# Performance work log

Measured on AMD Instinct MI355X. Metric: run time of the kernel, lower is better.

Reference implementation:

```python
import jax, jax.numpy as jnp
import numpy as np

N_NODES = 50000
N_EDGES = 800000
D = 96        # node feature dim (init arg D)
C = 16        # number of classes
BN_EPS = 1e-5


def _mlp_layer(x, w, b, g, beta):
    # Linear -> ReLU -> BatchNorm1d (training-mode batch stats, biased var)
    h = jax.nn.relu(x @ w + b)
    mu = h.mean(axis=0)
    var = h.var(axis=0)
    return g * (h - mu) * jax.lax.rsqrt(var + BN_EPS) + beta


def _gine_conv(x, e, src, dst, w, b, g, beta):
    # PyG GINEConv (eps=0): nn((1+eps)*x + sum_j ReLU(x_j + e_ij))
    msg = jax.nn.relu(x[src] + e)                      # [E, D] gather + edge add
    agg = jax.ops.segment_sum(msg, dst, num_segments=N_NODES)  # scatter-add
    return _mlp_layer(x + agg, w, b, g, beta)


def setup_inputs() -> dict:
    ks = jax.random.split(jax.random.key(0), 16)

    def p(k, shape, fan_in):
        return jax.random.normal(k, shape, jnp.float32) * (1.0 / np.sqrt(fan_in))

    inp = {
        "x": jax.random.normal(ks[0], (N_NODES, D), jnp.float32),
        "edge_attr": jax.random.normal(ks[1], (N_EDGES, 1), jnp.float32),
        "edge_index": jax.random.randint(ks[2], (2, N_EDGES), 0, N_NODES, jnp.int32),
        # fresh Linear(1, D) applied to edge_attr in forward
        "lin_w": p(ks[3], (1, D), 1), "lin_b": jnp.zeros((D,), jnp.float32),
        # conv1: GINEConv(MLP([D, D]))
        "conv1_w": p(ks[4], (D, D), D), "conv1_b": jnp.zeros((D,), jnp.float32),
        "conv1_g": jnp.ones((D,), jnp.float32), "conv1_beta": jnp.zeros((D,), jnp.float32),
        # conv2: GINEConv(MLP([D, 64]))
        "conv2_w": p(ks[5], (D, 64), D), "conv2_b": jnp.zeros((64,), jnp.float32),
        "conv2_g": jnp.ones((64,), jnp.float32), "conv2_beta": jnp.zeros((64,), jnp.float32),
        # lin1: MLP([D+64, 96])
        "lin1_w": p(ks[6], (D + 64, 96), D + 64), "lin1_b": jnp.zeros((96,), jnp.float32),
        "lin1_g": jnp.ones((96,), jnp.float32), "lin1_beta": jnp.zeros((96,), jnp.float32),
        # mlp1: MLP([96, 96, C]) -> two Linear+ReLU+BN layers
        "mlp1a_w": p(ks[7], (96, 96), 96), "mlp1a_b": jnp.zeros((96,), jnp.float32),
        "mlp1a_g": jnp.ones((96,), jnp.float32), "mlp1a_beta": jnp.zeros((96,), jnp.float32),
        "mlp1b_w": p(ks[8], (96, C), 96), "mlp1b_b": jnp.zeros((C,), jnp.float32),
        "mlp1b_g": jnp.ones((C,), jnp.float32), "mlp1b_beta": jnp.zeros((C,), jnp.float32),
    }
    return inp


def reference(x, edge_attr, edge_index,
              lin_w, lin_b,
              conv1_w, conv1_b, conv1_g, conv1_beta,
              conv2_w, conv2_b, conv2_g, conv2_beta,
              lin1_w, lin1_b, lin1_g, lin1_beta,
              mlp1a_w, mlp1a_b, mlp1a_g, mlp1a_beta,
              mlp1b_w, mlp1b_b, mlp1b_g, mlp1b_beta):
    src, dst = edge_index[0], edge_index[1]
    # D_n(=96) > D_e(=1): edge_attr lifted to [E, D] by Linear(1, D)
    e = edge_attr @ lin_w + lin_b                      # [E, D]
    x1 = _gine_conv(x, e, src, dst, conv1_w, conv1_b, conv1_g, conv1_beta)   # [N, D]
    x2 = _gine_conv(x1, e, src, dst, conv2_w, conv2_b, conv2_g, conv2_beta)  # [N, 64]
    h = _mlp_layer(jnp.concatenate([x1, x2], axis=1), lin1_w, lin1_b, lin1_g, lin1_beta)  # [N, 96]
    # task='node', G=0 -> no pooling, no global features
    h = _mlp_layer(h, mlp1a_w, mlp1a_b, mlp1a_g, mlp1a_beta)
    out = _mlp_layer(h, mlp1b_w, mlp1b_b, mlp1b_g, mlp1b_beta)               # [N, C]
    return out
```

## Files before the change

### kernel.cpp

```cpp
#include <hip/hip_runtime.h>

#define NN 50000
#define NE 800000
#define DD 96
#define BN_EPS 1e-5
#define NB 196

typedef __attribute__((ext_vector_type(8))) short short8v;
typedef __attribute__((ext_vector_type(4))) float float4v;

__device__ inline float bf2f(unsigned u) { return __uint_as_float(u << 16); }
__device__ inline unsigned short f2bf(float f) {
  unsigned u = __float_as_uint(f);
  return (unsigned short)((u + 0x7FFF + ((u >> 16) & 1)) >> 16);
}
__device__ inline void unpack8(uint4 v, float* f) {
  f[0] = bf2f(v.x & 0xffff); f[1] = bf2f(v.x >> 16);
  f[2] = bf2f(v.y & 0xffff); f[3] = bf2f(v.y >> 16);
  f[4] = bf2f(v.z & 0xffff); f[5] = bf2f(v.z >> 16);
  f[6] = bf2f(v.w & 0xffff); f[7] = bf2f(v.w >> 16);
}
__device__ inline uint4 pack8(const float* f) {
  uint4 v;
  v.x = (unsigned)f2bf(f[0]) | ((unsigned)f2bf(f[1]) << 16);
  v.y = (unsigned)f2bf(f[2]) | ((unsigned)f2bf(f[3]) << 16);
  v.z = (unsigned)f2bf(f[4]) | ((unsigned)f2bf(f[5]) << 16);
  v.w = (unsigned)f2bf(f[6]) | ((unsigned)f2bf(f[7]) << 16);
  return v;
}

__global__ __launch_bounds__(256) void f2bf_k(const float* __restrict__ in,
                                              unsigned short* __restrict__ out,
                                              int n8) {
  int t = blockIdx.x * 256 + threadIdx.x;
  if (t >= n8) return;
  const float4* p = (const float4*)in + 2 * t;
  float4 a = p[0], b = p[1];
  float f[8] = {a.x, a.y, a.z, a.w, b.x, b.y, b.z, b.w};
  ((uint4*)out)[t] = pack8(f);
}

__global__ __launch_bounds__(256) void hist_rank(const int* __restrict__ dst,
                                                 int* __restrict__ counts,
                                                 int* __restrict__ rank) {
  int e = blockIdx.x * 256 + threadIdx.x;
  if (e < NE) rank[e] = atomicAdd(&counts[dst[e]], 1);
}

__global__ __launch_bounds__(256) void scan_part(const int* __restrict__ counts,
                                                 int* __restrict__ bsum) {
  __shared__ int s[256];
  int tid = threadIdx.x;
  int i = blockIdx.x * 256 + tid;
  s[tid] = (i < NN) ? counts[i] : 0;
  __syncthreads();
  for (int st = 128; st > 0; st >>= 1) {
    if (tid < st) s[tid] += s[tid + st];
    __syncthreads();
  }
  if (tid == 0) bsum[blockIdx.x] = s[0];
}

__global__ __launch_bounds__(256) void scan_top(const int* __restrict__ bsum,
                                                int* __restrict__ boff) {
  __shared__ int s[256];
  int tid = threadIdx.x;
  int v = (tid < NB) ? bsum[tid] : 0;
  s[tid] = v;
  __syncthreads();
  for (int off = 1; off < 256; off <<= 1) {
    int t = (tid >= off) ? s[tid - off] : 0;
    __syncthreads();
    s[tid] += t;
    __syncthreads();
  }
  if (tid < NB) boff[tid] = s[tid] - v;
}

__global__ __launch_bounds__(256) void scan_apply(
    const int* __restrict__ counts, const int* __restrict__ boff,
    int* __restrict__ rowstart) {
  __shared__ int s[256];
  int tid = threadIdx.x;
  int i = blockIdx.x * 256 + tid;
  int v = (i < NN) ? counts[i] : 0;
  s[tid] = v;
  __syncthreads();
  for (int off = 1; off < 256; off <<= 1) {
    int t = (tid >= off) ? s[tid - off] : 0;
    __syncthreads();
    s[tid] += t;
    __syncthreads();
  }
  if (i < NN) rowstart[i] = boff[blockIdx.x] + s[tid] - v;
  if (i == 0) rowstart[NN] = NE;
}

__global__ __launch_bounds__(256) void scatter_k(
    const int* __restrict__ src, const int* __restrict__ dst,
    const float* __restrict__ ea, const int* __restrict__ rowstart,
    const int* __restrict__ rank, unsigned* __restrict__ pack) {
  int e = blockIdx.x * 256 + threadIdx.x;
  if (e >= NE) return;
  int p = rowstart[dst[e]] + rank[e];
  pack[p] = (unsigned)src[e] | ((unsigned)f2bf(ea[e]) << 16);
}

__global__ __launch_bounds__(256) void agg_wave(
    const unsigned short* __restrict__ xin, const float* __restrict__ lw,
    const float* __restrict__ lb, const int* __restrict__ rowstart,
    const unsigned* __restrict__ pack, unsigned short* __restrict__ out) {
  int n = blockIdx.x * 4 + (threadIdx.x >> 6);
  int lane = threadIdx.x & 63;
  int es = lane / 12;
  int c8 = lane - es * 12;
  float lwv[8], lbv[8], acc[8];
#pragma unroll
  for (int i = 0; i < 8; i++) {
    lwv[i] = lw[c8 * 8 + i];
    lbv[i] = lb[c8 * 8 + i];
    acc[i] = 0.f;
  }
  if (es == 0) {
    uint4 xo = *(const uint4*)(xin + (size_t)n * DD + c8 * 8);
    unpack8(xo, acc);
  }
  int beg = rowstart[n], end = rowstart[n + 1];
  if (lane < 60) {
    int i = beg + es;
    for (; i + 5 < end; i += 10) {
      unsigned pk0 = pack[i], pk1 = pack[i + 5];
      float ev0 = bf2f(pk0 >> 16), ev1 = bf2f(pk1 >> 16);
      uint4 xv0 = *(const uint4*)(xin + (size_t)(pk0 & 0xffff) * DD + c8 * 8);
      uint4 xv1 = *(const uint4*)(xin + (size_t)(pk1 & 0xffff) * DD + c8 * 8);
      float xs0[8], xs1[8];
      unpack8(xv0, xs0);
      unpack8(xv1, xs1);
#pragma unroll
      for (int j = 0; j < 8; j++) {
        acc[j] += fmaxf(xs0[j] + fmaf(ev0, lwv[j], lbv[j]), 0.0f);
        acc[j] += fmaxf(xs1[j] + fmaf(ev1, lwv[j], lbv[j]), 0.0f);
      }
    }
    if (i < end) {
      unsigned pk = pack[i];
      float ev = bf2f(pk >> 16);
      uint4 xv = *(const uint4*)(xin + (size_t)(pk & 0xffff) * DD + c8 * 8);
      float xs[8];
      unpack8(xv, xs);
#pragma unroll
      for (int j = 0; j < 8; j++)
        acc[j] += fmaxf(xs[j] + fmaf(ev, lwv[j], lbv[j]), 0.0f);
    }
  }
#pragma unroll
  for (int j = 0; j < 8; j++) {
    float a = acc[j];
    float t1 = __shfl_down(a, 12);
    float t2 = __shfl_down(a, 24);
    float t3 = __shfl_down(a, 36);
    float t4 = __shfl_down(a, 48);
    acc[j] = a + t1 + t2 + t3 + t4;
  }
  if (es == 0)
    *(uint4*)(out + (size_t)n * DD + c8 * 8) = pack8(acc);
}

__global__ __launch_bounds__(256) void agg_wave_norm(
    const unsigned short* __restrict__ h, const double* __restrict__ st,
    const float* __restrict__ g, const float* __restrict__ be,
    const float* __restrict__ lw, const float* __restrict__ lb,
    const int* __restrict__ rowstart, const unsigned* __restrict__ pack,
    unsigned short* __restrict__ out) {
  __shared__ float scs[96], shs[96];
  int tid = threadIdx.x;
  if (tid < 96) {
    double mu = st[tid] / (double)NN;
    double var = st[96 + tid] / (double)NN - mu * mu;
    double inv = 1.0 / sqrt(var + (double)BN_EPS);
    double sc = (double)g[tid] * inv;
    scs[tid] = (float)sc;
    shs[tid] = (float)((double)be[tid] - mu * sc);
  }
  __syncthreads();
  int n = blockIdx.x * 4 + (tid >> 6);
  int lane = tid & 63;
  int es = lane / 12;
  int c8 = lane - es * 12;
  float sc[8], tsh[8], tlb[8], lwv[8], acc[8];
#pragma unroll
  for (int i = 0; i < 8; i++) {
    sc[i] = scs[c8 * 8 + i];
    tsh[i] = shs[c8 * 8 + i];
    tlb[i] = tsh[i] + lb[c8 * 8 + i];
    lwv[i] = lw[c8 * 8 + i];
    acc[i] = 0.f;
  }
  if (es == 0) {
    uint4 xo = *(const uint4*)(h + (size_t)n * DD + c8 * 8);
    float f[8];
    unpack8(xo, f);
#pragma unroll
    for (int i = 0; i < 8; i++) acc[i] = fmaf(sc[i], f[i], tsh[i]);
  }
  int beg = rowstart[n], end = rowstart[n + 1];
  if (lane < 60) {
    int i = beg + es;
    for (; i + 5 < end; i += 10) {
      unsigned pk0 = pack[i], pk1 = pack[i + 5];
      float ev0 = bf2f(pk0 >> 16), ev1 = bf2f(pk1 >> 16);
      uint4 xv0 = *(const uint4*)(h + (size_t)(pk0 & 0xffff) * DD + c8 * 8);
      uint4 xv1 = *(const uint4*)(h + (size_t)(pk1 & 0xffff) * DD + c8 * 8);
      float xs0[8], xs1[8];
      unpack8(xv0, xs0);
      unpack8(xv1, xs1);
#pragma unroll
      for (int j = 0; j < 8; j++) {
        acc[j] += fmaxf(fmaf(sc[j], xs0[j], fmaf(ev0, lwv[j], tlb[j])), 0.0f);
        acc[j] += fmaxf(fmaf(sc[j], xs1[j], fmaf(ev1, lwv[j], tlb[j])), 0.0f);
      }
    }
    if (i < end) {
      unsigned pk = pack[i];
      float ev = bf2f(pk >> 16);
      uint4 xv = *(const uint4*)(h + (size_t)(pk & 0xffff) * DD + c8 * 8);
      float xs[8];
      unpack8(xv, xs);
#pragma unroll
      for (int j = 0; j < 8; j++)
        acc[j] += fmaxf(fmaf(sc[j], xs[j], fmaf(ev, lwv[j], tlb[j])), 0.0f);
    }
  }
#pragma unroll
  for (int j = 0; j < 8; j++) {
    float a = acc[j];
    float t1 = __shfl_down(a, 12);
    float t2 = __shfl_down(a, 24);
    float t3 = __shfl_down(a, 36);
    float t4 = __shfl_down(a, 48);
    acc[j] = a + t1 + t2 + t3 + t4;
  }
  if (es == 0)
    *(uint4*)(out + (size_t)n * DD + c8 * 8) = pack8(acc);
}

template <int K, int M, int KA, int KB>
__global__ __launch_bounds__(256) void wprep(
    const float* __restrict__ W, const float* __restrict__ b,
    const double* __restrict__ stA, const float* __restrict__ gA,
    const float* __restrict__ beA, const double* __restrict__ stB,
    const float* __restrict__ gB, const float* __restrict__ beB,
    unsigned short* __restrict__ Wz, float* __restrict__ bf) {
  constexpr int KT = K / 32, MT = M / 16;
  __shared__ float scA[KA > 0 ? KA : 1], shA[KA > 0 ? KA : 1];
  __shared__ float scB[KB > 0 ? KB : 1], shB[KB > 0 ? KB : 1];
  int tid = threadIdx.x;
  if (KA > 0 && tid < KA) {
    double mu = stA[tid] / (double)NN;
    double var = stA[KA + tid] / (double)NN - mu * mu;
    double inv = 1.0 / sqrt(var + (double)BN_EPS);
    double sc = (double)gA[tid] * inv;
    scA[tid] = (float)sc;
    shA[tid] = (float)((double)beA[tid] - mu * sc);
  }
  if (KB > 0 && tid < KB) {
    double mu = stB[tid] / (double)NN;
    double var = stB[KB + tid] / (double)NN - mu * mu;
    double inv = 1.0 / sqrt(var + (double)BN_EPS);
    double sc = (double)gB[tid] * inv;
    scB[tid] = (float)sc;
    shB[tid] = (float)((double)beB[tid] - mu * sc);
  }
  if (KA > 0 || KB > 0) __syncthreads();

  int t = blockIdx.x * 256 + tid;
  if (t < KT * MT * 64) {
    int lane = t & 63, fr = t >> 6;
    int kt = fr / MT, ct = fr - kt * MT;
    int col = ct * 16 + (lane & 15);
    int k0 = kt * 32 + (lane >> 4) * 8;
    float f[8];
#pragma unroll
    for (int j = 0; j < 8; j++) {
      int k = k0 + j;
      float w = W[k * M + col];
      if (KA > 0 && k < KA) w *= scA[k];
      if (KB > 0 && k >= KA && k < KA + KB) w *= scB[k - KA];
      f[j] = w;
    }
    ((uint4*)Wz)[t] = pack8(f);
  } else if (t < KT * MT * 64 + M) {
    int j = t - KT * MT * 64;
    float acc = b[j];
    if (KA > 0)
      for (int k = 0; k < KA; k++) acc += shA[k] * W[k * M + j];
    if (KB > 0)
      for (int k = 0; k < KB; k++) acc += shB[k] * W[(KA + k) * M + j];
    bf[j] = acc;
  }
}

template <int K1, int K2, int M, bool OUTF32>
__global__ __launch_bounds__(256) void gemm_mfma(
    const unsigned short* __restrict__ A1,
    const unsigned short* __restrict__ A2,
    const unsigned short* __restrict__ Wz, const float* __restrict__ bias,
    void* __restrict__ hOut, double* __restrict__ stats) {
  constexpr int K = K1 + K2;
  constexpr int KT = K / 32;
  constexpr int MT = M / 16;
  constexpr int NT = NN / 16;
  int tid = threadIdx.x;
  int wave = tid >> 6, lane = tid & 63;
  int lr = lane & 15, lk = lane >> 4;

  float bj[MT], s[MT], q[MT];
#pragma unroll
  for (int ct = 0; ct < MT; ct++) {
    bj[ct] = bias[ct * 16 + lr];
    s[ct] = 0.f;
    q[ct] = 0.f;
  }

  for (int tt = blockIdx.x * 4 + wave; tt < NT; tt += gridDim.x * 4) {
    float4v acc[MT];
#pragma unroll
    for (int ct = 0; ct < MT; ct++) acc[ct] = (float4v){0.f, 0.f, 0.f, 0.f};

    const unsigned short* a1 = A1 + (size_t)(tt * 16 + lr) * K1 + lk * 8;
    const unsigned short* a2 =
        (K2 > 0) ? A2 + (size_t)(tt * 16 + lr) * K2 + lk * 8 : a1;
#pragma unroll
    for (int kt = 0; kt < KT; kt++) {
      short8v av;
      if (kt * 32 < K1)
        av = *reinterpret_cast<const short8v*>(a1 + kt * 32);
      else
        av = *reinterpret_cast<const short8v*>(a2 + (kt * 32 - K1));
#pragma unroll
      for (int ct = 0; ct < MT; ct++) {
        short8v bv = *reinterpret_cast<const short8v*>(
            Wz + ((size_t)(kt * MT + ct) * 64 + lane) * 8);
        acc[ct] =
            __builtin_amdgcn_mfma_f32_16x16x32_bf16(av, bv, acc[ct], 0, 0, 0);
      }
    }
#pragma unroll
    for (int ct = 0; ct < MT; ct++) {
#pragma unroll
      for (int i = 0; i < 4; i++) {
        float o = fmaxf(acc[ct][i] + bj[ct], 0.f);
        size_t row = (size_t)tt * 16 + lk * 4 + i;
        if (OUTF32)
          ((float*)hOut)[row * M + ct * 16 + lr] = o;
        else
          ((unsigned short*)hOut)[row * M + ct * 16 + lr] = f2bf(o);
        s[ct] += o;
        q[ct] += o * o;
      }
    }
  }

  __shared__ float sred[4][M], qred[4][M];
#pragma unroll
  for (int ct = 0; ct < MT; ct++) {
    float ss = s[ct], qq = q[ct];
    ss += __shfl_xor(ss, 16);
    ss += __shfl_xor(ss, 32);
    qq += __shfl_xor(qq, 16);
    qq += __shfl_xor(qq, 32);
    if (lk == 0) {
      sred[wave][ct * 16 + lr] = ss;
      qred[wave][ct * 16 + lr] = qq;
    }
  }
  __syncthreads();
  if (tid < M) {
    double ss = (double)sred[0][tid] + sred[1][tid] + sred[2][tid] + sred[3][tid];
    double qq = (double)qred[0][tid] + qred[1][tid] + qred[2][tid] + qred[3][tid];
    atomicAdd(&stats[tid], ss);
    atomicAdd(&stats[M + tid], qq);
  }
}

__global__ __launch_bounds__(256) void bnout(const float4* __restrict__ h,
                                             const double* __restrict__ stats,
                                             const float* __restrict__ g,
                                             const float* __restrict__ beta,
                                             float4* __restrict__ out) {
  __shared__ float sc[16], sh[16];
  int tid = threadIdx.x;
  if (tid < 16) {
    double mu = stats[tid] / (double)NN;
    double var = stats[16 + tid] / (double)NN - mu * mu;
    double inv = 1.0 / sqrt(var + (double)BN_EPS);
    double scale = (double)g[tid] * inv;
    sc[tid] = (float)scale;
    sh[tid] = (float)((double)beta[tid] - mu * scale);
  }
  __syncthreads();
  int t = blockIdx.x * 256 + tid;
  if (t >= NN * 4) return;
  float4 v = h[t];
  int j0 = (4 * t) & 15;
  float4 o;
  o.x = fmaf(v.x, sc[j0 + 0], sh[j0 + 0]);
  o.y = fmaf(v.y, sc[j0 + 1], sh[j0 + 1]);
  o.z = fmaf(v.z, sc[j0 + 2], sh[j0 + 2]);
  o.w = fmaf(v.w, sc[j0 + 3], sh[j0 + 3]);
  out[t] = o;
}

static inline char* alignup(char* p, size_t a) {
  return (char*)(((uintptr_t)p + a - 1) & ~(uintptr_t)(a - 1));
}

extern "C" void kernel_launch(void* const* d_in, const int* in_sizes, int n_in,
                              void* d_out, int out_size, void* d_ws,
                              size_t ws_size, hipStream_t stream) {
  const float* x = (const float*)d_in[0];
  const float* ea = (const float*)d_in[1];
  const int* ei = (const int*)d_in[2];
  const int* src = ei;
  const int* dst = ei + NE;
  const float* lin_w = (const float*)d_in[3];
  const float* lin_b = (const float*)d_in[4];
  const float* c1_w = (const float*)d_in[5];
  const float* c1_b = (const float*)d_in[6];
  const float* c1_g = (const float*)d_in[7];
  const float* c1_be = (const float*)d_in[8];
  const float* c2_w = (const float*)d_in[9];
  const float* c2_b = (const float*)d_in[10];
  const float* c2_g = (const float*)d_in[11];
  const float* c2_be = (const float*)d_in[12];
  const float* l1_w = (const float*)d_in[13];
  const float* l1_b = (const float*)d_in[14];
  const float* l1_g = (const float*)d_in[15];
  const float* l1_be = (const float*)d_in[16];
  const float* ma_w = (const float*)d_in[17];
  const float* ma_b = (const float*)d_in[18];
  const float* ma_g = (const float*)d_in[19];
  const float* ma_be = (const float*)d_in[20];
  const float* mb_w = (const float*)d_in[21];
  const float* mb_b = (const float*)d_in[22];
  const float* mb_g = (const float*)d_in[23];
  const float* mb_be = (const float*)d_in[24];

  typedef unsigned short us;
  char* p = (char*)d_ws;
  us* xb = (us*)p;   p += (size_t)NN * 96 * 2;
  us* Ab = (us*)p;   p += (size_t)NN * 96 * 2;
  us* H1 = (us*)p;   p += (size_t)NN * 96 * 2;
  us* H2 = (us*)p;   p += (size_t)NN * 64 * 2;
  us* H3 = (us*)p;   p += (size_t)NN * 96 * 2;
  us* H4 = (us*)p;   p += (size_t)NN * 96 * 2;
  float* H5 = (float*)p; p += (size_t)NN * 16 * 4;
  p = alignup(p, 256);
  us* Wz1 = (us*)p;  p += 3 * 6 * 64 * 8 * 2;
  us* Wz2 = (us*)p;  p += 3 * 4 * 64 * 8 * 2;
  us* Wz3 = (us*)p;  p += 5 * 6 * 64 * 8 * 2;
  us* Wz4 = (us*)p;  p += 3 * 6 * 64 * 8 * 2;
  us* Wz5 = (us*)p;  p += 3 * 1 * 64 * 8 * 2;
  p = alignup(p, 256);
  float* bf1 = (float*)p; p += 96 * 4;
  float* bf2 = (float*)p; p += 64 * 4;
  float* bf3 = (float*)p; p += 96 * 4;
  float* bf4 = (float*)p; p += 96 * 4;
  float* bf5 = (float*)p; p += 16 * 4;
  p = alignup(p, 256);
  char* zbase = p;
  int* counts = (int*)p;  p += (size_t)NN * 4;
  double* stats = (double*)p; p += (size_t)5 * 192 * 8;
  size_t zbytes = (size_t)(p - zbase);
  int* rowstart = (int*)p; p += (size_t)(NN + 1) * 4;
  int* bsum = (int*)p;    p += 256 * 4;
  int* boff = (int*)p;    p += 256 * 4;
  int* rank = (int*)p;    p += (size_t)NE * 4;
  unsigned* pack = (unsigned*)p; p += (size_t)NE * 4;

  hipMemsetAsync(zbase, 0, zbytes, stream);

  const int eb = (NE + 255) / 256;
  const int n12 = NN * 12;
  const int b12 = (n12 + 255) / 256;
  const int aggG = NN / 4;
  const int GG = 782;

  f2bf_k<<<b12, 256, 0, stream>>>(x, xb, n12);
  hist_rank<<<eb, 256, 0, stream>>>(dst, counts, rank);
  scan_part<<<NB, 256, 0, stream>>>(counts, bsum);
  scan_top<<<1, 256, 0, stream>>>(bsum, boff);
  scan_apply<<<NB, 256, 0, stream>>>(counts, boff, rowstart);
  scatter_k<<<eb, 256, 0, stream>>>(src, dst, ea, rowstart, rank, pack);

  agg_wave<<<aggG, 256, 0, stream>>>(xb, lin_w, lin_b, rowstart, pack, Ab);
  wprep<96, 96, 0, 0><<<5, 256, 0, stream>>>(
      c1_w, c1_b, nullptr, nullptr, nullptr, nullptr, nullptr, nullptr, Wz1,
      bf1);
  gemm_mfma<96, 0, 96, false><<<GG, 256, 0, stream>>>(Ab, nullptr, Wz1, bf1,
                                                      H1, stats);

  agg_wave_norm<<<aggG, 256, 0, stream>>>(H1, stats, c1_g, c1_be, lin_w, lin_b,
                                          rowstart, pack, Ab);
  wprep<96, 64, 0, 0><<<4, 256, 0, stream>>>(
      c2_w, c2_b, nullptr, nullptr, nullptr, nullptr, nullptr, nullptr, Wz2,
      bf2);
  gemm_mfma<96, 0, 64, false><<<GG, 256, 0, stream>>>(Ab, nullptr, Wz2, bf2,
                                                      H2, stats + 192);

  wprep<160, 96, 96, 64><<<8, 256, 0, stream>>>(l1_w, l1_b, stats, c1_g, c1_be,
                                                stats + 192, c2_g, c2_be, Wz3,
                                                bf3);
  gemm_mfma<96, 64, 96, false><<<GG, 256, 0, stream>>>(H1, H2, Wz3, bf3, H3,
                                                       stats + 384);

  wprep<96, 96, 96, 0><<<5, 256, 0, stream>>>(ma_w, ma_b, stats + 384, l1_g,
                                              l1_be, nullptr, nullptr, nullptr,
                                              Wz4, bf4);
  gemm_mfma<96, 0, 96, false><<<GG, 256, 0, stream>>>(H3, nullptr, Wz4, bf4,
                                                      H4, stats + 576);

  wprep<96, 16, 96, 0><<<1, 256, 0, stream>>>(mb_w, mb_b, stats + 576, ma_g,
                                              ma_be, nullptr, nullptr, nullptr,
                                              Wz5, bf5);
  gemm_mfma<96, 0, 16, true><<<GG, 256, 0, stream>>>(H4, nullptr, Wz5, bf5, H5,
                                                     stats + 768);
  bnout<<<(NN * 4 + 255) / 256, 256, 0, stream>>>(
      (const float4*)H5, stats + 768, mb_g, mb_be, (float4*)d_out);
}
```

Baseline: 369.7 us.

## Replace double atomic BN stats with per-block partials and a reduction kernel

```diff
diff --git a/kernel.cpp b/kernel.cpp
--- a/kernel.cpp
+++ b/kernel.cpp
@@ -5,6 +5,7 @@
 #define DD 96
 #define BN_EPS 1e-5
 #define NB 196
+#define GGEMM 782
 
 typedef __attribute__((ext_vector_type(8))) short short8v;
 typedef __attribute__((ext_vector_type(4))) float float4v;
@@ -167,31 +168,19 @@
 }
 
 __global__ __launch_bounds__(256) void agg_wave_norm(
-    const unsigned short* __restrict__ h, const double* __restrict__ st,
-    const float* __restrict__ g, const float* __restrict__ be,
+    const unsigned short* __restrict__ h, const float* __restrict__ coeff,
     const float* __restrict__ lw, const float* __restrict__ lb,
     const int* __restrict__ rowstart, const unsigned* __restrict__ pack,
     unsigned short* __restrict__ out) {
-  __shared__ float scs[96], shs[96];
-  int tid = threadIdx.x;
-  if (tid < 96) {
-    double mu = st[tid] / (double)NN;
-    double var = st[96 + tid] / (double)NN - mu * mu;
-    double inv = 1.0 / sqrt(var + (double)BN_EPS);
-    double sc = (double)g[tid] * inv;
-    scs[tid] = (float)sc;
-    shs[tid] = (float)((double)be[tid] - mu * sc);
-  }
-  __syncthreads();
-  int n = blockIdx.x * 4 + (tid >> 6);
-  int lane = tid & 63;
+  int n = blockIdx.x * 4 + (threadIdx.x >> 6);
+  int lane = threadIdx.x & 63;
   int es = lane / 12;
   int c8 = lane - es * 12;
   float sc[8], tsh[8], tlb[8], lwv[8], acc[8];
 #pragma unroll
   for (int i = 0; i < 8; i++) {
-    sc[i] = scs[c8 * 8 + i];
-    tsh[i] = shs[c8 * 8 + i];
+    sc[i] = coeff[c8 * 8 + i];
+    tsh[i] = coeff[96 + c8 * 8 + i];
     tlb[i] = tsh[i] + lb[c8 * 8 + i];
     lwv[i] = lw[c8 * 8 + i];
     acc[i] = 0.f;
@@ -245,35 +234,14 @@
 }
 
 template <int K, int M, int KA, int KB>
-__global__ __launch_bounds__(256) void wprep(
-    const float* __restrict__ W, const float* __restrict__ b,
-    const double* __restrict__ stA, const float* __restrict__ gA,
-    const float* __restrict__ beA, const double* __restrict__ stB,
-    const float* __restrict__ gB, const float* __restrict__ beB,
-    unsigned short* __restrict__ Wz, float* __restrict__ bf) {
+__global__ __launch_bounds__(256) void wprep(const float* __restrict__ W,
+                                             const float* __restrict__ b,
+                                             const float* __restrict__ cA,
+                                             const float* __restrict__ cB,
+                                             unsigned short* __restrict__ Wz,
+                                             float* __restrict__ bf) {
   constexpr int KT = K / 32, MT = M / 16;
-  __shared__ float scA[KA > 0 ? KA : 1], shA[KA > 0 ? KA : 1];
-  __shared__ float scB[KB > 0 ? KB : 1], shB[KB > 0 ? KB : 1];
-  int tid = threadIdx.x;
-  if (KA > 0 && tid < KA) {
-    double mu = stA[tid] / (double)NN;
-    double var = stA[KA + tid] / (double)NN - mu * mu;
-    double inv = 1.0 / sqrt(var + (double)BN_EPS);
-    double sc = (double)gA[tid] * inv;
-    scA[tid] = (float)sc;
-    shA[tid] = (float)((double)beA[tid] - mu * sc);
-  }
-  if (KB > 0 && tid < KB) {
-    double mu = stB[tid] / (double)NN;
-    double var = stB[KB + tid] / (double)NN - mu * mu;
-    double inv = 1.0 / sqrt(var + (double)BN_EPS);
-    double sc = (double)gB[tid] * inv;
-    scB[tid] = (float)sc;
-    shB[tid] = (float)((double)beB[tid] - mu * sc);
-  }
-  if (KA > 0 || KB > 0) __syncthreads();
-
-  int t = blockIdx.x * 256 + tid;
+  int t = blockIdx.x * 256 + threadIdx.x;
   if (t < KT * MT * 64) {
     int lane = t & 63, fr = t >> 6;
     int kt = fr / MT, ct = fr - kt * MT;
@@ -284,8 +252,8 @@
     for (int j = 0; j < 8; j++) {
       int k = k0 + j;
       float w = W[k * M + col];
-      if (KA > 0 && k < KA) w *= scA[k];
-      if (KB > 0 && k >= KA && k < KA + KB) w *= scB[k - KA];
+      if (KA > 0 && k < KA) w *= cA[k];
+      if (KB > 0 && k >= KA && k < KA + KB) w *= cB[k - KA];
       f[j] = w;
     }
     ((uint4*)Wz)[t] = pack8(f);
@@ -293,9 +261,9 @@
     int j = t - KT * MT * 64;
     float acc = b[j];
     if (KA > 0)
-      for (int k = 0; k < KA; k++) acc += shA[k] * W[k * M + j];
+      for (int k = 0; k < KA; k++) acc += cA[KA + k] * W[k * M + j];
     if (KB > 0)
-      for (int k = 0; k < KB; k++) acc += shB[k] * W[(KA + k) * M + j];
+      for (int k = 0; k < KB; k++) acc += cB[KB + k] * W[(KA + k) * M + j];
     bf[j] = acc;
   }
 }
@@ -305,7 +273,7 @@
     const unsigned short* __restrict__ A1,
     const unsigned short* __restrict__ A2,
     const unsigned short* __restrict__ Wz, const float* __restrict__ bias,
-    void* __restrict__ hOut, double* __restrict__ stats) {
+    void* __restrict__ hOut, float* __restrict__ partial) {
   constexpr int K = K1 + K2;
   constexpr int KT = K / 32;
   constexpr int MT = M / 16;
@@ -376,38 +344,50 @@
   }
   __syncthreads();
   if (tid < M) {
-    double ss = (double)sred[0][tid] + sred[1][tid] + sred[2][tid] + sred[3][tid];
-    double qq = (double)qred[0][tid] + qred[1][tid] + qred[2][tid] + qred[3][tid];
-    atomicAdd(&stats[tid], ss);
-    atomicAdd(&stats[M + tid], qq);
+    partial[(size_t)blockIdx.x * (2 * M) + tid] =
+        sred[0][tid] + sred[1][tid] + sred[2][tid] + sred[3][tid];
+  } else if (tid < 2 * M) {
+    int j = tid - M;
+    partial[(size_t)blockIdx.x * (2 * M) + tid] =
+        qred[0][j] + qred[1][j] + qred[2][j] + qred[3][j];
+  }
+}
+
+template <int M>
+__global__ __launch_bounds__(256) void bn_red(const float* __restrict__ partial,
+                                              const float* __restrict__ g,
+                                              const float* __restrict__ beta,
+                                              float* __restrict__ coeff) {
+  __shared__ double dsum[2 * M];
+  int tid = threadIdx.x;
+  if (tid < 2 * M) {
+    double a = 0.0;
+    for (int b = 0; b < GGEMM; b++) a += partial[(size_t)b * (2 * M) + tid];
+    dsum[tid] = a;
+  }
+  __syncthreads();
+  if (tid < M) {
+    double mu = dsum[tid] / (double)NN;
+    double var = dsum[M + tid] / (double)NN - mu * mu;
+    double inv = 1.0 / sqrt(var + (double)BN_EPS);
+    double sc = (double)g[tid] * inv;
+    coeff[tid] = (float)sc;
+    coeff[M + tid] = (float)((double)beta[tid] - mu * sc);
   }
 }
 
 __global__ __launch_bounds__(256) void bnout(const float4* __restrict__ h,
-                                             const double* __restrict__ stats,
-                                             const float* __restrict__ g,
-                                             const float* __restrict__ beta,
+                                             const float* __restrict__ coeff,
                                              float4* __restrict__ out) {
-  __shared__ float sc[16], sh[16];
-  int tid = threadIdx.x;
-  if (tid < 16) {
-    double mu = stats[tid] / (double)NN;
-    double var = stats[16 + tid] / (double)NN - mu * mu;
-    double inv = 1.0 / sqrt(var + (double)BN_EPS);
-    double scale = (double)g[tid] * inv;
-    sc[tid] = (float)scale;
-    sh[tid] = (float)((double)beta[tid] - mu * scale);
-  }
-  __syncthreads();
-  int t = blockIdx.x * 256 + tid;
+  int t = blockIdx.x * 256 + threadIdx.x;
   if (t >= NN * 4) return;
   float4 v = h[t];
   int j0 = (4 * t) & 15;
   float4 o;
-  o.x = fmaf(v.x, sc[j0 + 0], sh[j0 + 0]);
-  o.y = fmaf(v.y, sc[j0 + 1], sh[j0 + 1]);
-  o.z = fmaf(v.z, sc[j0 + 2], sh[j0 + 2]);
-  o.w = fmaf(v.w, sc[j0 + 3], sh[j0 + 3]);
+  o.x = fmaf(v.x, coeff[j0 + 0], coeff[16 + j0 + 0]);
+  o.y = fmaf(v.y, coeff[j0 + 1], coeff[16 + j0 + 1]);
+  o.z = fmaf(v.z, coeff[j0 + 2], coeff[16 + j0 + 2]);
+  o.w = fmaf(v.w, coeff[j0 + 3], coeff[16 + j0 + 3]);
   out[t] = o;
 }
 
@@ -467,10 +447,16 @@
   float* bf3 = (float*)p; p += 96 * 4;
   float* bf4 = (float*)p; p += 96 * 4;
   float* bf5 = (float*)p; p += 16 * 4;
+  float* co1 = (float*)p; p += 192 * 4;
+  float* co2 = (float*)p; p += 128 * 4;
+  float* co3 = (float*)p; p += 192 * 4;
+  float* co4 = (float*)p; p += 192 * 4;
+  float* co5 = (float*)p; p += 32 * 4;
+  p = alignup(p, 256);
+  float* partial = (float*)p; p += (size_t)GGEMM * 192 * 4;
   p = alignup(p, 256);
   char* zbase = p;
   int* counts = (int*)p;  p += (size_t)NN * 4;
-  double* stats = (double*)p; p += (size_t)5 * 192 * 8;
   size_t zbytes = (size_t)(p - zbase);
   int* rowstart = (int*)p; p += (size_t)(NN + 1) * 4;
   int* bsum = (int*)p;    p += 256 * 4;
@@ -484,7 +470,6 @@
   const int n12 = NN * 12;
   const int b12 = (n12 + 255) / 256;
   const int aggG = NN / 4;
-  const int GG = 782;
 
   f2bf_k<<<b12, 256, 0, stream>>>(x, xb, n12);
   hist_rank<<<eb, 256, 0, stream>>>(dst, counts, rank);
@@ -494,37 +479,37 @@
   scatter_k<<<eb, 256, 0, stream>>>(src, dst, ea, rowstart, rank, pack);
 
   agg_wave<<<aggG, 256, 0, stream>>>(xb, lin_w, lin_b, rowstart, pack, Ab);
-  wprep<96, 96, 0, 0><<<5, 256, 0, stream>>>(
-      c1_w, c1_b, nullptr, nullptr, nullptr, nullptr, nullptr, nullptr, Wz1,
-      bf1);
-  gemm_mfma<96, 0, 96, false><<<GG, 256, 0, stream>>>(Ab, nullptr, Wz1, bf1,
-                                                      H1, stats);
-
-  agg_wave_norm<<<aggG, 256, 0, stream>>>(H1, stats, c1_g, c1_be, lin_w, lin_b,
-                                          rowstart, pack, Ab);
-  wprep<96, 64, 0, 0><<<4, 256, 0, stream>>>(
-      c2_w, c2_b, nullptr, nullptr, nullptr, nullptr, nullptr, nullptr, Wz2,
-      bf2);
-  gemm_mfma<96, 0, 64, false><<<GG, 256, 0, stream>>>(Ab, nullptr, Wz2, bf2,
-                                                      H2, stats + 192);
-
-  wprep<160, 96, 96, 64><<<8, 256, 0, stream>>>(l1_w, l1_b, stats, c1_g, c1_be,
-                                                stats + 192, c2_g, c2_be, Wz3,
+  wprep<96, 96, 0, 0><<<5, 256, 0, stream>>>(c1_w, c1_b, nullptr, nullptr, Wz1,
+                                             bf1);
+  gemm_mfma<96, 0, 96, false><<<GGEMM, 256, 0, stream>>>(Ab, nullptr, Wz1, bf1,
+                                                         H1, partial);
+  bn_red<96><<<1, 256, 0, stream>>>(partial, c1_g, c1_be, co1);
+
+  agg_wave_norm<<<aggG, 256, 0, stream>>>(H1, co1, lin_w, lin_b, rowstart,
+                                          pack, Ab);
+  wprep<96, 64, 0, 0><<<4, 256, 0, stream>>>(c2_w, c2_b, nullptr, nullptr, Wz2,
+                                             bf2);
+  gemm_mfma<96, 0, 64, false><<<GGEMM, 256, 0, stream>>>(Ab, nullptr, Wz2, bf2,
+                                                         H2, partial);
+  bn_red<64><<<1, 256, 0, stream>>>(partial, c2_g, c2_be, co2);
+
+  wprep<160, 96, 96, 64><<<8, 256, 0, stream>>>(l1_w, l1_b, co1, co2, Wz3,
                                                 bf3);
-  gemm_mfma<96, 64, 96, false><<<GG, 256, 0, stream>>>(H1, H2, Wz3, bf3, H3,
-                                                       stats + 384);
-
-  wprep<96, 96, 96, 0><<<5, 256, 0, stream>>>(ma_w, ma_b, stats + 384, l1_g,
-                                              l1_be, nullptr, nullptr, nullptr,
-                                              Wz4, bf4);
-  gemm_mfma<96, 0, 96, false><<<GG, 256, 0, stream>>>(H3, nullptr, Wz4, bf4,
-                                                      H4, stats + 576);
-
-  wprep<96, 16, 96, 0><<<1, 256, 0, stream>>>(mb_w, mb_b, stats + 576, ma_g,
-                                              ma_be, nullptr, nullptr, nullptr,
-                                              Wz5, bf5);
-  gemm_mfma<96, 0, 16, true><<<GG, 256, 0, stream>>>(H4, nullptr, Wz5, bf5, H5,
-                                                     stats + 768);
-  bnout<<<(NN * 4 + 255) / 256, 256, 0, stream>>>(
-      (const float4*)H5, stats + 768, mb_g, mb_be, (float4*)d_out);
-}
+  gemm_mfma<96, 64, 96, false><<<GGEMM, 256, 0, stream>>>(H1, H2, Wz3, bf3, H3,
+                                                          partial);
+  bn_red<96><<<1, 256, 0, stream>>>(partial, l1_g, l1_be, co3);
+
+  wprep<96, 96, 96, 0><<<5, 256, 0, stream>>>(ma_w, ma_b, co3, nullptr, Wz4,
+                                              bf4);
+  gemm_mfma<96, 0, 96, false><<<GGEMM, 256, 0, stream>>>(H3, nullptr, Wz4, bf4,
+                                                         H4, partial);
+  bn_red<96><<<1, 256, 0, stream>>>(partial, ma_g, ma_be, co4);
+
+  wprep<96, 16, 96, 0><<<1, 256, 0, stream>>>(mb_w, mb_b, co4, nullptr, Wz5,
+                                              bf5);
+  gemm_mfma<96, 0, 16, true><<<GGEMM, 256, 0, stream>>>(H4, nullptr, Wz5, bf5,
+                                                        H5, partial);
+  bn_red<16><<<1, 256, 0, stream>>>(partial, mb_g, mb_be, co5);
+  bnout<<<(NN * 4 + 255) / 256, 256, 0, stream>>>((const float4*)H5, co5,
+                                                  (float4*)d_out);
+}
```

Measured after the change: 635.5 us. +71.9%, slower.
